# Performance work log

Hardware: AMD Instinct MI355X
Metric: run time of the kernel (lower is better)

Reference implementation:

```python
import jax, jax.numpy as jnp
import numpy as np

EPS_COS = 1e-8  # torch cosine_similarity eps
EPS_LN = 1e-5   # torch LayerNorm eps


def setup_inputs() -> dict:
    key = jax.random.key(0)
    ks = jax.random.split(key, 8)
    B, N, D, C = 256, 65536, 1024, 103
    s = 1.0 / np.sqrt(D)
    return {
        "visual_input": jnp.zeros((1,), jnp.float32),
        "query_input": jax.random.normal(ks[0], (B, D), jnp.float32),
        "memory_keys": jax.random.normal(ks[1], (N, D), jnp.float32),
        "W_enc": jax.random.normal(ks[2], (D, D), jnp.float32) * s,
        "b_enc": jnp.zeros((D,), jnp.float32),
        "W_d": jax.random.normal(ks[3], (D, D), jnp.float32) * s,
        "b_d": jnp.zeros((D,), jnp.float32),
        "ln_g": jnp.ones((D,), jnp.float32),
        "ln_b": jnp.zeros((D,), jnp.float32),
        "W_cls": jax.random.normal(ks[4], (C, 2 * D), jnp.float32) * (1.0 / np.sqrt(2 * D)),
        "b_cls": jnp.zeros((C,), jnp.float32),
        "k": 32,
    }


def reference(visual_input, query_input, memory_keys, W_enc, b_enc, W_d, b_d,
              ln_g, ln_b, W_cls, b_cls, k):
    # visual encoder + relu -> query embedding [B, D]
    q = jax.nn.relu(query_input @ W_enc.T + b_enc)
    # cosine-similarity kNN over memory bank [N, D]
    qn = q / jnp.maximum(jnp.linalg.norm(q, axis=-1, keepdims=True), EPS_COS)
    mn = memory_keys / jnp.maximum(jnp.linalg.norm(memory_keys, axis=-1, keepdims=True), EPS_COS)
    sim = qn @ mn.T                      # [B, N]
    _, idx = jax.lax.top_k(sim, k)       # [B, k]
    mk = memory_keys[idx]                # [B, k, D] gather
    # memory attention
    qt = jax.nn.relu(q @ W_d.T + b_d)    # [B, D]
    scores = jnp.einsum('bd,bkd->bk', qt, mk)
    w = jax.nn.softmax(scores, axis=-1)
    attended = jnp.einsum('bk,bkd->bd', w, mk)
    x = attended + q
    mu = jnp.mean(x, axis=-1, keepdims=True)
    var = jnp.mean((x - mu) ** 2, axis=-1, keepdims=True)
    ma_out = (x - mu) * jax.lax.rsqrt(var + EPS_LN) * ln_g + ln_b
    # classifier on concatenated features
    merged = jnp.concatenate([q, ma_out], axis=1)  # [B, 2D]
    return merged @ W_cls.T + b_cls
```

## Files before the change

### kernel.cpp

```cpp
#include <hip/hip_runtime.h>
#include <stdint.h>

typedef unsigned short u16;
typedef unsigned int u32;
typedef __attribute__((ext_vector_type(2))) float f32x2;
typedef __attribute__((ext_vector_type(4))) float f32x4;
typedef __attribute__((ext_vector_type(4))) u32 u32x4;
typedef __attribute__((ext_vector_type(2))) u32 u32x2;
typedef __attribute__((ext_vector_type(8))) short bf16x8;

#define NKEYS 65536
#define DIM 1024
#define BQ 256
#define NCLS 103
#define NCAND 64
#define SROW 40

__device__ __forceinline__ u16 f2bf(float x) {
  u32 u = __float_as_uint(x);
  u = u + 0x7FFFu + ((u >> 16) & 1u);
  return (u16)(u >> 16);
}
__device__ __forceinline__ u32 cvtpk(float lo, float hi) {
  u32 d;
  asm("v_cvt_pk_bf16_f32 %0, %1, %2" : "=v"(d) : "v"(lo), "v"(hi));
  return d;
}

__global__ __launch_bounds__(256) void gemm_nt_f32(
    const float* __restrict__ A, const float* __restrict__ B,
    float* __restrict__ partial)
{
  __shared__ float sAT[2][16][68];
  __shared__ float sBT[2][16][68];
  const int tid = threadIdx.x;
  const int n0 = blockIdx.x * 64;
  const int m0 = blockIdx.y * 64;
  const int kz = blockIdx.z;
  const int r = tid & 63, kq = tid >> 6;
  const int tx = tid & 15, ty = tid >> 4;
  float acc[4][4] = {};

  const float* ag = A + (size_t)(m0 + r) * DIM + kz * 256 + kq * 4;
  const float* bg = B + (size_t)(n0 + r) * DIM + kz * 256 + kq * 4;

  f32x4 av = *(const f32x4*)(ag);
  f32x4 bv = *(const f32x4*)(bg);
#pragma unroll
  for (int i = 0; i < 4; ++i) {
    sAT[0][kq * 4 + i][r] = av[i];
    sBT[0][kq * 4 + i][r] = bv[i];
  }
  __syncthreads();

  for (int kb = 0; kb < 16; ++kb) {
    const int cur = kb & 1;
    if (kb + 1 < 16) {
      av = *(const f32x4*)(ag + (kb + 1) * 16);
      bv = *(const f32x4*)(bg + (kb + 1) * 16);
    }
#pragma unroll
    for (int kk = 0; kk < 16; ++kk) {
      const f32x4 a4 = *(const f32x4*)&sAT[cur][kk][ty * 4];
      const f32x4 b4 = *(const f32x4*)&sBT[cur][kk][tx * 4];
#pragma unroll
      for (int i = 0; i < 4; ++i)
#pragma unroll
        for (int j = 0; j < 4; ++j) acc[i][j] += a4[i] * b4[j];
    }
    if (kb + 1 < 16) {
#pragma unroll
      for (int i = 0; i < 4; ++i) {
        sAT[cur ^ 1][kq * 4 + i][r] = av[i];
        sBT[cur ^ 1][kq * 4 + i][r] = bv[i];
      }
    }
    __syncthreads();
  }
#pragma unroll
  for (int i = 0; i < 4; ++i) {
    f32x4 ov = {acc[i][0], acc[i][1], acc[i][2], acc[i][3]};
    *(f32x4*)(partial + (size_t)kz * 262144u + (size_t)(m0 + ty * 4 + i) * DIM + n0 + tx * 4) = ov;
  }
}

__global__ __launch_bounds__(256) void reduce_bias_relu(
    const float* __restrict__ partial, const float* __restrict__ bias,
    float* __restrict__ outf, u16* __restrict__ outb, const int wbf)
{
  const int i4 = blockIdx.x * 256 + threadIdx.x;
  const int e = i4 * 4;
  const int n = e & (DIM - 1);
  f32x4 s = *(const f32x4*)(partial + e);
  s += *(const f32x4*)(partial + 262144u + e);
  s += *(const f32x4*)(partial + 2u * 262144u + e);
  s += *(const f32x4*)(partial + 3u * 262144u + e);
  s += *(const f32x4*)(bias + n);
#pragma unroll
  for (int i = 0; i < 4; ++i) s[i] = fmaxf(s[i], 0.f);
  *(f32x4*)(outf + e) = s;
  if (wbf) {
    u32x2 h = {cvtpk(s[0], s[1]), cvtpk(s[2], s[3])};
    *(u32x2*)(outb + e) = h;
  }
}

__global__ __launch_bounds__(512) void simgemm(
    const float* __restrict__ keys, const u16* __restrict__ qb,
    u16* __restrict__ sim)
{
  __shared__ u16 sA[2][256 * SROW];
  __shared__ u16 sB[2][128 * SROW];
  __shared__ float snorm[128];
  const int tid = threadIdx.x;
  const int n0 = blockIdx.x * 128;

  const int a_r = tid >> 1;
  const int a_h = (tid & 1) * 16;
  const u16* agp = qb + (size_t)a_r * DIM + a_h;
  const int a_ws = a_r * SROW + a_h;

  const int b_r = tid >> 2;
  const int b_q = (tid & 3) * 8;
  const float* bgp = keys + (size_t)(n0 + b_r) * DIM + b_q;
  const int b_ws = b_r * SROW + b_q;

  const int lane = tid & 63, wave = tid >> 6;
  const int wm = (wave >> 1) * 64;
  const int wn = (wave & 1) * 64;
  const int lr = lane & 15;
  const int lk = (lane >> 4) * 8;
  const int l4 = (lane >> 4) * 4;

  float nrm = 0.f;
  f32x4 acc[4][4];
#pragma unroll
  for (int i = 0; i < 4; ++i)
#pragma unroll
    for (int j = 0; j < 4; ++j) acc[i][j] = (f32x4){0.f, 0.f, 0.f, 0.f};

  f32x4 b00, b01, b10, b11, b20, b21, b30, b31;
  u32x4 a00, a01, a10, a11;

#define LOADB(B0, B1, T) do { \
    B0 = *(const f32x4*)(bgp + (size_t)(T) * 32); \
    B1 = *(const f32x4*)(bgp + (size_t)(T) * 32 + 4); \
  } while (0)
#define LOADA(A0, A1, T) do { \
    A0 = *(const u32x4*)(agp + (size_t)(T) * 32); \
    A1 = *(const u32x4*)(agp + (size_t)(T) * 32 + 8); \
  } while (0)
#define WRITE(B0, B1, A0, A1, BUF) do { \
    nrm += B0[0]*B0[0] + B0[1]*B0[1] + B0[2]*B0[2] + B0[3]*B0[3]; \
    nrm += B1[0]*B1[0] + B1[1]*B1[1] + B1[2]*B1[2] + B1[3]*B1[3]; \
    u32x4 bp; \
    bp.x = cvtpk(B0[0], B0[1]); bp.y = cvtpk(B0[2], B0[3]); \
    bp.z = cvtpk(B1[0], B1[1]); bp.w = cvtpk(B1[2], B1[3]); \
    *(u32x4*)&sB[BUF][b_ws] = bp; \
    *(u32x4*)&sA[BUF][a_ws] = A0; \
    *(u32x4*)&sA[BUF][a_ws + 8] = A1; \
  } while (0)
#define COMPUTE(BUF) do { \
    bf16x8 af[4], bfr[4]; \
    _Pragma("unroll") \
    for (int f = 0; f < 4; ++f) { \
      af[f]  = *(const bf16x8*)&sA[BUF][(wm + f * 16 + lr) * SROW + lk]; \
      bfr[f] = *(const bf16x8*)&sB[BUF][(wn + f * 16 + lr) * SROW + lk]; \
    } \
    _Pragma("unroll") \
    for (int i = 0; i < 4; ++i) \
      _Pragma("unroll") \
      for (int j = 0; j < 4; ++j) \
        acc[i][j] = __builtin_amdgcn_mfma_f32_16x16x32_bf16(af[i], bfr[j], acc[i][j], 0, 0, 0); \
  } while (0)

  LOADB(b00, b01, 0); LOADB(b10, b11, 1); LOADB(b20, b21, 2); LOADB(b30, b31, 3);
  LOADA(a00, a01, 0); LOADA(a10, a11, 1);
  WRITE(b00, b01, a00, a01, 0);
  __syncthreads();

  for (int tt = 0; tt < 32; tt += 4) {
    if (tt + 4 < 32) LOADB(b00, b01, tt + 4);
    LOADA(a00, a01, tt + 2);
    COMPUTE(0);
    WRITE(b10, b11, a10, a11, 1);
    __syncthreads();
    if (tt + 5 < 32) LOADB(b10, b11, tt + 5);
    LOADA(a10, a11, tt + 3);
    COMPUTE(1);
    WRITE(b20, b21, a00, a01, 0);
    __syncthreads();
    if (tt + 6 < 32) LOADB(b20, b21, tt + 6);
    if (tt + 4 < 32) LOADA(a00, a01, tt + 4);
    COMPUTE(0);
    WRITE(b30, b31, a10, a11, 1);
    __syncthreads();
    if (tt + 7 < 32) LOADB(b30, b31, tt + 7);
    if (tt + 5 < 32) LOADA(a10, a11, tt + 5);
    COMPUTE(1);
    if (tt + 4 < 32) WRITE(b00, b01, a00, a01, 0);
    __syncthreads();
  }
#undef LOADB
#undef LOADA
#undef WRITE
#undef COMPUTE

  nrm += __shfl_xor(nrm, 1);
  nrm += __shfl_xor(nrm, 2);
  if ((tid & 3) == 0) snorm[b_r] = nrm;
  __syncthreads();

#pragma unroll
  for (int j = 0; j < 4; ++j) {
    const int nl = wn + j * 16 + lr;
    const float scl = 1.f / fmaxf(sqrtf(snorm[nl]), 1e-8f);
    const size_t ng = (size_t)(n0 + nl);
#pragma unroll
    for (int i = 0; i < 4; ++i) {
      const int mb = wm + i * 16 + l4;
#pragma unroll
      for (int r = 0; r < 4; ++r) {
        sim[(size_t)(mb + r) * NKEYS + ng] = f2bf(acc[i][j][r] * scl);
      }
    }
  }
}

__global__ __launch_bounds__(512) void select_attn_cls(
    const u16* __restrict__ sim, const float* __restrict__ keys,
    const float* __restrict__ q, const float* __restrict__ qt,
    const float* __restrict__ ln_g, const float* __restrict__ ln_b,
    const float* __restrict__ Wc, const float* __restrict__ bc,
    float* __restrict__ out)
{
  __shared__ int redc[8];
  __shared__ int sc1, sc2;
  __shared__ int clist[NCAND];
  __shared__ float sdq[NCAND], sdqt[NCAND], snr[NCAND];
  __shared__ int srowi[32];
  __shared__ float sw[32];
  __shared__ float red1[8], red2[8];
  __shared__ float smg[2048];
  const int tid = threadIdx.x, lane = tid & 63, wave = tid >> 6;
  const int m = blockIdx.x;

  const u32x4* row = (const u32x4*)(sim + (size_t)m * NKEYS);
  u32 ku[16][4];
#pragma unroll
  for (int i = 0; i < 16; ++i) {
    const u32x4 v = row[i * 512 + tid];
#pragma unroll
    for (int c = 0; c < 4; ++c) {
      u32 lo = v[c] & 0xFFFFu, hi = v[c] >> 16;
      lo ^= (lo & 0x8000u) ? 0xFFFFu : 0x8000u;
      hi ^= (hi & 0x8000u) ? 0xFFFFu : 0x8000u;
      ku[i][c] = lo | (hi << 16);
    }
  }
  int lo_b = 0, hi_b = 65536;
  while (hi_b - lo_b > 1) {
    const u32 mid = (u32)((lo_b + hi_b) >> 1);
    int c = 0;
#pragma unroll
    for (int i = 0; i < 16; ++i)
#pragma unroll
      for (int k = 0; k < 4; ++k) {
        const u32 x = ku[i][k];
        c += ((x & 0xFFFFu) >= mid) ? 1 : 0;
        c += ((x >> 16) >= mid) ? 1 : 0;
      }
#pragma unroll
    for (int j = 32; j; j >>= 1) c += __shfl_xor(c, j);
    if ((tid & 63) == 0) redc[tid >> 6] = c;
    __syncthreads();
    int tot = 0;
#pragma unroll
    for (int w = 0; w < 8; ++w) tot += redc[w];
    if (tot >= NCAND) lo_b = (int)mid; else hi_b = (int)mid;
    __syncthreads();
  }
  const u32 tau = (u32)lo_b;

  int ch = 0;
#pragma unroll
  for (int i = 0; i < 16; ++i)
#pragma unroll
    for (int k = 0; k < 4; ++k) {
      const u32 x = ku[i][k];
      ch += ((x & 0xFFFFu) > tau) ? 1 : 0;
      ch += ((x >> 16) > tau) ? 1 : 0;
    }
#pragma unroll
  for (int j = 32; j; j >>= 1) ch += __shfl_xor(ch, j);
  if ((tid & 63) == 0) redc[tid >> 6] = ch;
  if (tid == 0) { sc1 = 0; sc2 = 0; }
  __syncthreads();
  int nhi = 0;
#pragma unroll
  for (int w = 0; w < 8; ++w) nhi += redc[w];

#pragma unroll
  for (int i = 0; i < 16; ++i)
#pragma unroll
    for (int k = 0; k < 4; ++k) {
      const int nb = (i * 512 + tid) * 8 + k * 2;
      const u32 x = ku[i][k];
      const u32 l = x & 0xFFFFu, h = x >> 16;
      if (l > tau) { int p = atomicAdd(&sc1, 1); clist[p] = nb; }
      else if (l == tau) { int p = atomicAdd(&sc2, 1); if (nhi + p < NCAND) clist[nhi + p] = nb; }
      if (h > tau) { int p = atomicAdd(&sc1, 1); clist[p] = nb + 1; }
      else if (h == tau) { int p = atomicAdd(&sc2, 1); if (nhi + p < NCAND) clist[nhi + p] = nb + 1; }
    }
  __syncthreads();

  f32x4 q4[4], qt4[4];
#pragma unroll
  for (int i = 0; i < 4; ++i) {
    q4[i]  = *(const f32x4*)(q  + (size_t)m * DIM + i * 256 + lane * 4);
    qt4[i] = *(const f32x4*)(qt + (size_t)m * DIM + i * 256 + lane * 4);
  }
  for (int ci = 0; ci < 8; ++ci) {
    const int c = wave * 8 + ci;
    const float* kr = keys + (size_t)clist[c] * DIM;
    float dq = 0.f, dt = 0.f, ss = 0.f;
#pragma unroll
    for (int i = 0; i < 4; ++i) {
      const f32x4 kv = *(const f32x4*)(kr + i * 256 + lane * 4);
#pragma unroll
      for (int e = 0; e < 4; ++e) {
        dq += kv[e] * q4[i][e];
        dt += kv[e] * qt4[i][e];
        ss += kv[e] * kv[e];
      }
    }
#pragma unroll
    for (int j = 32; j; j >>= 1) {
      dq += __shfl_xor(dq, j);
      dt += __shfl_xor(dt, j);
      ss += __shfl_xor(ss, j);
    }
    if (lane == 0) { sdq[c] = dq; sdqt[c] = dt; snr[c] = ss; }
  }
  __syncthreads();

  if (wave == 0) {
    float v = sdq[lane] / fmaxf(sqrtf(snr[lane]), 1e-8f);
    int p = lane;
#pragma unroll
    for (int k = 2; k <= 64; k <<= 1)
#pragma unroll
      for (int j = k >> 1; j > 0; j >>= 1) {
        const float ov = __shfl_xor(v, j);
        const int op = __shfl_xor(p, j);
        const bool tl = ((lane & j) == 0) == ((lane & k) == 0);
        const bool take = tl ? (ov > v) : (ov < v);
        if (take) { v = ov; p = op; }
      }
    float sc = (lane < 32) ? sdqt[p] : -3.4e38f;
    float mx = sc;
#pragma unroll
    for (int j = 16; j; j >>= 1) mx = fmaxf(mx, __shfl_xor(mx, j));
    const float e = (lane < 32) ? expf(sc - mx) : 0.f;
    float s = e;
#pragma unroll
    for (int j = 16; j; j >>= 1) s += __shfl_xor(s, j);
    if (lane < 32) { sw[lane] = e / s; srowi[lane] = clist[p]; }
  }
  __syncthreads();

  const int d0 = tid * 2;
  f32x2 at = {0.f, 0.f};
  for (int j = 0; j < 32; ++j) {
    const float wj = sw[j];
    const f32x2 kv = *(const f32x2*)(keys + (size_t)srowi[j] * DIM + d0);
    at += wj * kv;
  }
  const f32x2 qv = *(const f32x2*)(q + (size_t)m * DIM + d0);
  const f32x2 x = at + qv;
  float s1 = x[0] + x[1];
#pragma unroll
  for (int j = 32; j; j >>= 1) s1 += __shfl_xor(s1, j);
  if (lane == 0) red1[wave] = s1;
  __syncthreads();
  float mu = 0.f;
#pragma unroll
  for (int w = 0; w < 8; ++w) mu += red1[w];
  mu *= (1.f / 1024.f);
  const f32x2 xc = x - mu;
  float s2 = xc[0] * xc[0] + xc[1] * xc[1];
#pragma unroll
  for (int j = 32; j; j >>= 1) s2 += __shfl_xor(s2, j);
  if (lane == 0) red2[wave] = s2;
  __syncthreads();
  float var = 0.f;
#pragma unroll
  for (int w = 0; w < 8; ++w) var += red2[w];
  var *= (1.f / 1024.f);
  const float rstd = rsqrtf(var + 1e-5f);
  const f32x2 g = *(const f32x2*)(ln_g + d0);
  const f32x2 b = *(const f32x2*)(ln_b + d0);
  const f32x2 ma = xc * rstd * g + b;
  *(f32x2*)&smg[d0] = qv;
  *(f32x2*)&smg[1024 + d0] = ma;
  __syncthreads();

  for (int c = wave; c < NCLS; c += 8) {
    const float* w = Wc + (size_t)c * 2048;
    float a = 0.f;
#pragma unroll
    for (int i = 0; i < 8; ++i) {
      const f32x4 wv = *(const f32x4*)(w + i * 256 + lane * 4);
      const f32x4 mv = *(const f32x4*)&smg[i * 256 + lane * 4];
#pragma unroll
      for (int e = 0; e < 4; ++e) a += wv[e] * mv[e];
    }
#pragma unroll
    for (int j = 32; j; j >>= 1) a += __shfl_xor(a, j);
    if (lane == 0) out[(size_t)m * NCLS + c] = a + bc[c];
  }
}

extern "C" void kernel_launch(void* const* d_in, const int* in_sizes, int n_in,
                              void* d_out, int out_size, void* d_ws, size_t ws_size,
                              hipStream_t stream)
{
  const float* query = (const float*)d_in[1];
  const float* keys  = (const float*)d_in[2];
  const float* Wenc  = (const float*)d_in[3];
  const float* benc  = (const float*)d_in[4];
  const float* Wd    = (const float*)d_in[5];
  const float* bd    = (const float*)d_in[6];
  const float* lng   = (const float*)d_in[7];
  const float* lnb   = (const float*)d_in[8];
  const float* Wcls  = (const float*)d_in[9];
  const float* bcls  = (const float*)d_in[10];
  float* out = (float*)d_out;
  char* ws = (char*)d_ws;

  float* q   = (float*)(ws + 0);
  float* qt  = (float*)(ws + 1048576u);
  u16*   qb  = (u16*)(ws + 2097152u);
  char*  big = ws + 2621440u;
  float* par = (float*)big;
  u16*   sim = (u16*)big;

  gemm_nt_f32<<<dim3(16, 4, 4), 256, 0, stream>>>(query, Wenc, par);
  reduce_bias_relu<<<256, 256, 0, stream>>>(par, benc, q, qb, 1);
  gemm_nt_f32<<<dim3(16, 4, 4), 256, 0, stream>>>(q, Wd, par);
  reduce_bias_relu<<<256, 256, 0, stream>>>(par, bd, qt, qb, 0);
  simgemm<<<dim3(512), 512, 0, stream>>>(keys, qb, sim);
  select_attn_cls<<<256, 512, 0, stream>>>(sim, keys, q, qt, lng, lnb, Wcls, bcls, out);
}
```

Before: 183.5 us.

## Fuse all stages into one persistent kernel with software grid barriers

```diff
diff --git a/kernel.cpp b/kernel.cpp
--- a/kernel.cpp
+++ b/kernel.cpp
@@ -11,10 +11,11 @@
 
 #define NKEYS 65536
 #define DIM 1024
-#define BQ 256
 #define NCLS 103
 #define NCAND 64
 #define SROW 40
+#define NBLK 256
+#define NTHR 512
 
 __device__ __forceinline__ u16 f2bf(float x) {
   u32 u = __float_as_uint(x);
@@ -27,120 +28,160 @@
   return d;
 }
 
-__global__ __launch_bounds__(256) void gemm_nt_f32(
-    const float* __restrict__ A, const float* __restrict__ B,
-    float* __restrict__ partial)
+union SMEM {
+  struct { float sAT[2][32][68]; float sBT[2][32][68]; } g;
+  struct { u16 sA[2][256 * SROW]; u16 sB[2][128 * SROW]; float snorm[128]; } s;
+  struct { int redc[8]; int sc1, sc2; int clist[NCAND];
+           float sdq[NCAND], sdqt[NCAND], snr[NCAND];
+           int srowi[32]; float sw[32]; float red1[8], red2[8];
+           float smg[2048]; } t;
+};
+
+__device__ __forceinline__ void gridbar(u32* cnt, u32* gen) {
+  __syncthreads();
+  if (threadIdx.x == 0) {
+    __threadfence();
+    u32 g0 = __hip_atomic_load(gen, __ATOMIC_RELAXED, __HIP_MEMORY_SCOPE_AGENT);
+    u32 old = __hip_atomic_fetch_add(cnt, 1u, __ATOMIC_ACQ_REL, __HIP_MEMORY_SCOPE_AGENT);
+    if (old == NBLK - 1u) {
+      __hip_atomic_store(cnt, 0u, __ATOMIC_RELAXED, __HIP_MEMORY_SCOPE_AGENT);
+      __hip_atomic_fetch_add(gen, 1u, __ATOMIC_ACQ_REL, __HIP_MEMORY_SCOPE_AGENT);
+    } else {
+      while (__hip_atomic_load(gen, __ATOMIC_ACQUIRE, __HIP_MEMORY_SCOPE_AGENT) == g0)
+        __builtin_amdgcn_s_sleep(2);
+    }
+    __threadfence();
+  }
+  __syncthreads();
+}
+
+__device__ __forceinline__ void small_gemm(const float* __restrict__ A,
+                                           const float* __restrict__ B,
+                                           float* __restrict__ partial,
+                                           SMEM* sm, int b, int tid) {
+  const int n0 = (b & 15) * 64;
+  const int m0 = ((b >> 4) & 3) * 64;
+  const int kz = (b >> 6) & 3;
+  const int ar = tid & 63;
+  const int kq = (tid >> 6) * 4;
+  const int tx = tid & 15, ty = tid >> 4;
+  float acc[2][4] = {};
+  const float* ag = A + (size_t)(m0 + ar) * DIM + kz * 256 + kq;
+  const float* bg = B + (size_t)(n0 + ar) * DIM + kz * 256 + kq;
+  f32x4 av = *(const f32x4*)ag;
+  f32x4 bv = *(const f32x4*)bg;
+#pragma unroll
+  for (int i = 0; i < 4; ++i) {
+    sm->g.sAT[0][kq + i][ar] = av[i];
+    sm->g.sBT[0][kq + i][ar] = bv[i];
+  }
+  __syncthreads();
+  for (int kb = 0; kb < 8; ++kb) {
+    const int cur = kb & 1;
+    if (kb + 1 < 8) {
+      av = *(const f32x4*)(ag + (kb + 1) * 32);
+      bv = *(const f32x4*)(bg + (kb + 1) * 32);
+    }
+#pragma unroll
+    for (int kk = 0; kk < 32; ++kk) {
+      const f32x2 a2 = *(const f32x2*)&sm->g.sAT[cur][kk][ty * 2];
+      const f32x4 b4 = *(const f32x4*)&sm->g.sBT[cur][kk][tx * 4];
+#pragma unroll
+      for (int i = 0; i < 2; ++i)
+#pragma unroll
+        for (int j = 0; j < 4; ++j) acc[i][j] += a2[i] * b4[j];
+    }
+    if (kb + 1 < 8) {
+#pragma unroll
+      for (int i = 0; i < 4; ++i) {
+        sm->g.sAT[cur ^ 1][kq + i][ar] = av[i];
+        sm->g.sBT[cur ^ 1][kq + i][ar] = bv[i];
+      }
+    }
+    __syncthreads();
+  }
+#pragma unroll
+  for (int i = 0; i < 2; ++i) {
+    f32x4 ov = {acc[i][0], acc[i][1], acc[i][2], acc[i][3]};
+    *(f32x4*)(partial + (size_t)kz * 262144u + (size_t)(m0 + ty * 2 + i) * DIM + n0 + tx * 4) = ov;
+  }
+}
+
+__device__ __forceinline__ void reduce_phase(const float* __restrict__ partial,
+                                             const float* __restrict__ bias,
+                                             float* __restrict__ outf,
+                                             u16* __restrict__ outb, int gid) {
+  if (gid < 65536) {
+    const int e = gid * 4;
+    const int n = e & (DIM - 1);
+    f32x4 s = *(const f32x4*)(partial + e);
+    s += *(const f32x4*)(partial + 262144u + e);
+    s += *(const f32x4*)(partial + 2u * 262144u + e);
+    s += *(const f32x4*)(partial + 3u * 262144u + e);
+    s += *(const f32x4*)(bias + n);
+#pragma unroll
+    for (int i = 0; i < 4; ++i) s[i] = fmaxf(s[i], 0.f);
+    *(f32x4*)(outf + e) = s;
+    if (outb) {
+      u32x2 h = {cvtpk(s[0], s[1]), cvtpk(s[2], s[3])};
+      *(u32x2*)(outb + e) = h;
+    }
+  }
+}
+
+__global__ __launch_bounds__(NTHR, 2) void mega(
+    const float* __restrict__ query, const float* __restrict__ keys,
+    const float* __restrict__ Wenc, const float* __restrict__ benc,
+    const float* __restrict__ Wd, const float* __restrict__ bd,
+    const float* __restrict__ lng, const float* __restrict__ lnb,
+    const float* __restrict__ Wc, const float* __restrict__ bc,
+    float* __restrict__ q, float* __restrict__ qt, u16* __restrict__ qb,
+    float* __restrict__ par1, float* __restrict__ par2, u16* __restrict__ sim,
+    u32* __restrict__ bar, float* __restrict__ out)
 {
-  __shared__ float sAT[2][16][68];
-  __shared__ float sBT[2][16][68];
+  __shared__ SMEM smem;
+  SMEM* const sm = &smem;
   const int tid = threadIdx.x;
-  const int n0 = blockIdx.x * 64;
-  const int m0 = blockIdx.y * 64;
-  const int kz = blockIdx.z;
-  const int r = tid & 63, kq = tid >> 6;
-  const int tx = tid & 15, ty = tid >> 4;
-  float acc[4][4] = {};
-
-  const float* ag = A + (size_t)(m0 + r) * DIM + kz * 256 + kq * 4;
-  const float* bg = B + (size_t)(n0 + r) * DIM + kz * 256 + kq * 4;
-
-  f32x4 av = *(const f32x4*)(ag);
-  f32x4 bv = *(const f32x4*)(bg);
-#pragma unroll
-  for (int i = 0; i < 4; ++i) {
-    sAT[0][kq * 4 + i][r] = av[i];
-    sBT[0][kq * 4 + i][r] = bv[i];
-  }
-  __syncthreads();
-
-  for (int kb = 0; kb < 16; ++kb) {
-    const int cur = kb & 1;
-    if (kb + 1 < 16) {
-      av = *(const f32x4*)(ag + (kb + 1) * 16);
-      bv = *(const f32x4*)(bg + (kb + 1) * 16);
-    }
-#pragma unroll
-    for (int kk = 0; kk < 16; ++kk) {
-      const f32x4 a4 = *(const f32x4*)&sAT[cur][kk][ty * 4];
-      const f32x4 b4 = *(const f32x4*)&sBT[cur][kk][tx * 4];
+  const int b = blockIdx.x;
+  const int lane = tid & 63, wave = tid >> 6;
+  u32* cnt = bar;
+  u32* gen = bar + 32;
+
+  small_gemm(query, Wenc, par1, sm, b, tid);
+  gridbar(cnt, gen);
+  reduce_phase(par1, benc, q, qb, b * NTHR + tid);
+  gridbar(cnt, gen);
+  small_gemm(q, Wd, par2, sm, b, tid);
+  gridbar(cnt, gen);
+  reduce_phase(par2, bd, qt, (u16*)0, b * NTHR + tid);
+  gridbar(cnt, gen);
+
+  {
+    const int a_r = tid >> 1;
+    const int a_h = (tid & 1) * 16;
+    const u16* agp = qb + (size_t)a_r * DIM + a_h;
+    const int a_ws = a_r * SROW + a_h;
+    const int b_r = tid >> 2;
+    const int b_q = (tid & 3) * 8;
+    const int b_ws = b_r * SROW + b_q;
+    const int wm = (wave >> 1) * 64;
+    const int wn = (wave & 1) * 64;
+    const int lr = lane & 15;
+    const int lk = (lane >> 4) * 8;
+    const int l4 = (lane >> 4) * 4;
+
+    for (int s = 0; s < 2; ++s) {
+      const int n0 = (b * 2 + s) * 128;
+      const float* bgp = keys + (size_t)(n0 + b_r) * DIM + b_q;
+      float nrm = 0.f;
+      f32x4 acc[4][4];
 #pragma unroll
       for (int i = 0; i < 4; ++i)
 #pragma unroll
-        for (int j = 0; j < 4; ++j) acc[i][j] += a4[i] * b4[j];
-    }
-    if (kb + 1 < 16) {
-#pragma unroll
-      for (int i = 0; i < 4; ++i) {
-        sAT[cur ^ 1][kq * 4 + i][r] = av[i];
-        sBT[cur ^ 1][kq * 4 + i][r] = bv[i];
-      }
-    }
-    __syncthreads();
-  }
-#pragma unroll
-  for (int i = 0; i < 4; ++i) {
-    f32x4 ov = {acc[i][0], acc[i][1], acc[i][2], acc[i][3]};
-    *(f32x4*)(partial + (size_t)kz * 262144u + (size_t)(m0 + ty * 4 + i) * DIM + n0 + tx * 4) = ov;
-  }
-}
-
-__global__ __launch_bounds__(256) void reduce_bias_relu(
-    const float* __restrict__ partial, const float* __restrict__ bias,
-    float* __restrict__ outf, u16* __restrict__ outb, const int wbf)
-{
-  const int i4 = blockIdx.x * 256 + threadIdx.x;
-  const int e = i4 * 4;
-  const int n = e & (DIM - 1);
-  f32x4 s = *(const f32x4*)(partial + e);
-  s += *(const f32x4*)(partial + 262144u + e);
-  s += *(const f32x4*)(partial + 2u * 262144u + e);
-  s += *(const f32x4*)(partial + 3u * 262144u + e);
-  s += *(const f32x4*)(bias + n);
-#pragma unroll
-  for (int i = 0; i < 4; ++i) s[i] = fmaxf(s[i], 0.f);
-  *(f32x4*)(outf + e) = s;
-  if (wbf) {
-    u32x2 h = {cvtpk(s[0], s[1]), cvtpk(s[2], s[3])};
-    *(u32x2*)(outb + e) = h;
-  }
-}
-
-__global__ __launch_bounds__(512) void simgemm(
-    const float* __restrict__ keys, const u16* __restrict__ qb,
-    u16* __restrict__ sim)
-{
-  __shared__ u16 sA[2][256 * SROW];
-  __shared__ u16 sB[2][128 * SROW];
-  __shared__ float snorm[128];
-  const int tid = threadIdx.x;
-  const int n0 = blockIdx.x * 128;
-
-  const int a_r = tid >> 1;
-  const int a_h = (tid & 1) * 16;
-  const u16* agp = qb + (size_t)a_r * DIM + a_h;
-  const int a_ws = a_r * SROW + a_h;
-
-  const int b_r = tid >> 2;
-  const int b_q = (tid & 3) * 8;
-  const float* bgp = keys + (size_t)(n0 + b_r) * DIM + b_q;
-  const int b_ws = b_r * SROW + b_q;
-
-  const int lane = tid & 63, wave = tid >> 6;
-  const int wm = (wave >> 1) * 64;
-  const int wn = (wave & 1) * 64;
-  const int lr = lane & 15;
-  const int lk = (lane >> 4) * 8;
-  const int l4 = (lane >> 4) * 4;
-
-  float nrm = 0.f;
-  f32x4 acc[4][4];
-#pragma unroll
-  for (int i = 0; i < 4; ++i)
-#pragma unroll
-    for (int j = 0; j < 4; ++j) acc[i][j] = (f32x4){0.f, 0.f, 0.f, 0.f};
-
-  f32x4 b00, b01, b10, b11, b20, b21, b30, b31;
-  u32x4 a00, a01, a10, a11;
+        for (int j = 0; j < 4; ++j) acc[i][j] = (f32x4){0.f, 0.f, 0.f, 0.f};
+
+      f32x4 b00, b01, b10, b11, b20, b21, b30, b31;
+      u32x4 a00, a01, a10, a11;
 
 #define LOADB(B0, B1, T) do { \
     B0 = *(const f32x4*)(bgp + (size_t)(T) * 32); \
@@ -156,16 +197,16 @@
     u32x4 bp; \
     bp.x = cvtpk(B0[0], B0[1]); bp.y = cvtpk(B0[2], B0[3]); \
     bp.z = cvtpk(B1[0], B1[1]); bp.w = cvtpk(B1[2], B1[3]); \
-    *(u32x4*)&sB[BUF][b_ws] = bp; \
-    *(u32x4*)&sA[BUF][a_ws] = A0; \
-    *(u32x4*)&sA[BUF][a_ws + 8] = A1; \
+    *(u32x4*)&sm->s.sB[BUF][b_ws] = bp; \
+    *(u32x4*)&sm->s.sA[BUF][a_ws] = A0; \
+    *(u32x4*)&sm->s.sA[BUF][a_ws + 8] = A1; \
   } while (0)
 #define COMPUTE(BUF) do { \
     bf16x8 af[4], bfr[4]; \
     _Pragma("unroll") \
     for (int f = 0; f < 4; ++f) { \
-      af[f]  = *(const bf16x8*)&sA[BUF][(wm + f * 16 + lr) * SROW + lk]; \
-      bfr[f] = *(const bf16x8*)&sB[BUF][(wn + f * 16 + lr) * SROW + lk]; \
+      af[f]  = *(const bf16x8*)&sm->s.sA[BUF][(wm + f * 16 + lr) * SROW + lk]; \
+      bfr[f] = *(const bf16x8*)&sm->s.sB[BUF][(wn + f * 16 + lr) * SROW + lk]; \
     } \
     _Pragma("unroll") \
     for (int i = 0; i < 4; ++i) \
@@ -174,250 +215,238 @@
         acc[i][j] = __builtin_amdgcn_mfma_f32_16x16x32_bf16(af[i], bfr[j], acc[i][j], 0, 0, 0); \
   } while (0)
 
-  LOADB(b00, b01, 0); LOADB(b10, b11, 1); LOADB(b20, b21, 2); LOADB(b30, b31, 3);
-  LOADA(a00, a01, 0); LOADA(a10, a11, 1);
-  WRITE(b00, b01, a00, a01, 0);
-  __syncthreads();
-
-  for (int tt = 0; tt < 32; tt += 4) {
-    if (tt + 4 < 32) LOADB(b00, b01, tt + 4);
-    LOADA(a00, a01, tt + 2);
-    COMPUTE(0);
-    WRITE(b10, b11, a10, a11, 1);
-    __syncthreads();
-    if (tt + 5 < 32) LOADB(b10, b11, tt + 5);
-    LOADA(a10, a11, tt + 3);
-    COMPUTE(1);
-    WRITE(b20, b21, a00, a01, 0);
-    __syncthreads();
-    if (tt + 6 < 32) LOADB(b20, b21, tt + 6);
-    if (tt + 4 < 32) LOADA(a00, a01, tt + 4);
-    COMPUTE(0);
-    WRITE(b30, b31, a10, a11, 1);
-    __syncthreads();
-    if (tt + 7 < 32) LOADB(b30, b31, tt + 7);
-    if (tt + 5 < 32) LOADA(a10, a11, tt + 5);
-    COMPUTE(1);
-    if (tt + 4 < 32) WRITE(b00, b01, a00, a01, 0);
-    __syncthreads();
-  }
+      LOADB(b00, b01, 0); LOADB(b10, b11, 1); LOADB(b20, b21, 2); LOADB(b30, b31, 3);
+      LOADA(a00, a01, 0); LOADA(a10, a11, 1);
+      WRITE(b00, b01, a00, a01, 0);
+      __syncthreads();
+
+      for (int tt = 0; tt < 32; tt += 4) {
+        if (tt + 4 < 32) LOADB(b00, b01, tt + 4);
+        LOADA(a00, a01, tt + 2);
+        COMPUTE(0);
+        WRITE(b10, b11, a10, a11, 1);
+        __syncthreads();
+        if (tt + 5 < 32) LOADB(b10, b11, tt + 5);
+        LOADA(a10, a11, tt + 3);
+        COMPUTE(1);
+        WRITE(b20, b21, a00, a01, 0);
+        __syncthreads();
+        if (tt + 6 < 32) LOADB(b20, b21, tt + 6);
+        if (tt + 4 < 32) LOADA(a00, a01, tt + 4);
+        COMPUTE(0);
+        WRITE(b30, b31, a10, a11, 1);
+        __syncthreads();
+        if (tt + 7 < 32) LOADB(b30, b31, tt + 7);
+        if (tt + 5 < 32) LOADA(a10, a11, tt + 5);
+        COMPUTE(1);
+        if (tt + 4 < 32) WRITE(b00, b01, a00, a01, 0);
+        __syncthreads();
+      }
 #undef LOADB
 #undef LOADA
 #undef WRITE
 #undef COMPUTE
 
-  nrm += __shfl_xor(nrm, 1);
-  nrm += __shfl_xor(nrm, 2);
-  if ((tid & 3) == 0) snorm[b_r] = nrm;
-  __syncthreads();
-
-#pragma unroll
-  for (int j = 0; j < 4; ++j) {
-    const int nl = wn + j * 16 + lr;
-    const float scl = 1.f / fmaxf(sqrtf(snorm[nl]), 1e-8f);
-    const size_t ng = (size_t)(n0 + nl);
-#pragma unroll
-    for (int i = 0; i < 4; ++i) {
-      const int mb = wm + i * 16 + l4;
-#pragma unroll
-      for (int r = 0; r < 4; ++r) {
-        sim[(size_t)(mb + r) * NKEYS + ng] = f2bf(acc[i][j][r] * scl);
-      }
-    }
-  }
-}
-
-__global__ __launch_bounds__(512) void select_attn_cls(
-    const u16* __restrict__ sim, const float* __restrict__ keys,
-    const float* __restrict__ q, const float* __restrict__ qt,
-    const float* __restrict__ ln_g, const float* __restrict__ ln_b,
-    const float* __restrict__ Wc, const float* __restrict__ bc,
-    float* __restrict__ out)
-{
-  __shared__ int redc[8];
-  __shared__ int sc1, sc2;
-  __shared__ int clist[NCAND];
-  __shared__ float sdq[NCAND], sdqt[NCAND], snr[NCAND];
-  __shared__ int srowi[32];
-  __shared__ float sw[32];
-  __shared__ float red1[8], red2[8];
-  __shared__ float smg[2048];
-  const int tid = threadIdx.x, lane = tid & 63, wave = tid >> 6;
-  const int m = blockIdx.x;
-
-  const u32x4* row = (const u32x4*)(sim + (size_t)m * NKEYS);
-  u32 ku[16][4];
-#pragma unroll
-  for (int i = 0; i < 16; ++i) {
-    const u32x4 v = row[i * 512 + tid];
-#pragma unroll
-    for (int c = 0; c < 4; ++c) {
-      u32 lo = v[c] & 0xFFFFu, hi = v[c] >> 16;
-      lo ^= (lo & 0x8000u) ? 0xFFFFu : 0x8000u;
-      hi ^= (hi & 0x8000u) ? 0xFFFFu : 0x8000u;
-      ku[i][c] = lo | (hi << 16);
-    }
-  }
-  int lo_b = 0, hi_b = 65536;
-  while (hi_b - lo_b > 1) {
-    const u32 mid = (u32)((lo_b + hi_b) >> 1);
-    int c = 0;
+      nrm += __shfl_xor(nrm, 1);
+      nrm += __shfl_xor(nrm, 2);
+      if ((tid & 3) == 0) sm->s.snorm[b_r] = nrm;
+      __syncthreads();
+
+#pragma unroll
+      for (int j = 0; j < 4; ++j) {
+        const int nl = wn + j * 16 + lr;
+        const float scl = 1.f / fmaxf(sqrtf(sm->s.snorm[nl]), 1e-8f);
+        const size_t ng = (size_t)(n0 + nl);
+#pragma unroll
+        for (int i = 0; i < 4; ++i) {
+          const int mb = wm + i * 16 + l4;
+#pragma unroll
+          for (int r = 0; r < 4; ++r) {
+            sim[(size_t)(mb + r) * NKEYS + ng] = f2bf(acc[i][j][r] * scl);
+          }
+        }
+      }
+      __syncthreads();
+    }
+  }
+  gridbar(cnt, gen);
+
+  {
+    const int m = b;
+    const u32x4* row = (const u32x4*)(sim + (size_t)m * NKEYS);
+    u32 ku[16][4];
+#pragma unroll
+    for (int i = 0; i < 16; ++i) {
+      const u32x4 v = row[i * 512 + tid];
+#pragma unroll
+      for (int c = 0; c < 4; ++c) {
+        u32 lo = v[c] & 0xFFFFu, hi = v[c] >> 16;
+        lo ^= (lo & 0x8000u) ? 0xFFFFu : 0x8000u;
+        hi ^= (hi & 0x8000u) ? 0xFFFFu : 0x8000u;
+        ku[i][c] = lo | (hi << 16);
+      }
+    }
+    int lo_b = 0, hi_b = 65536;
+    while (hi_b - lo_b > 1) {
+      const u32 mid = (u32)((lo_b + hi_b) >> 1);
+      int c = 0;
+#pragma unroll
+      for (int i = 0; i < 16; ++i)
+#pragma unroll
+        for (int k = 0; k < 4; ++k) {
+          const u32 x = ku[i][k];
+          c += ((x & 0xFFFFu) >= mid) ? 1 : 0;
+          c += ((x >> 16) >= mid) ? 1 : 0;
+        }
+#pragma unroll
+      for (int j = 32; j; j >>= 1) c += __shfl_xor(c, j);
+      if ((tid & 63) == 0) sm->t.redc[tid >> 6] = c;
+      __syncthreads();
+      int tot = 0;
+#pragma unroll
+      for (int w = 0; w < 8; ++w) tot += sm->t.redc[w];
+      if (tot >= NCAND) lo_b = (int)mid; else hi_b = (int)mid;
+      __syncthreads();
+    }
+    const u32 tau = (u32)lo_b;
+
+    int ch = 0;
 #pragma unroll
     for (int i = 0; i < 16; ++i)
 #pragma unroll
       for (int k = 0; k < 4; ++k) {
         const u32 x = ku[i][k];
-        c += ((x & 0xFFFFu) >= mid) ? 1 : 0;
-        c += ((x >> 16) >= mid) ? 1 : 0;
-      }
-#pragma unroll
-    for (int j = 32; j; j >>= 1) c += __shfl_xor(c, j);
-    if ((tid & 63) == 0) redc[tid >> 6] = c;
-    __syncthreads();
-    int tot = 0;
-#pragma unroll
-    for (int w = 0; w < 8; ++w) tot += redc[w];
-    if (tot >= NCAND) lo_b = (int)mid; else hi_b = (int)mid;
-    __syncthreads();
-  }
-  const u32 tau = (u32)lo_b;
-
-  int ch = 0;
-#pragma unroll
-  for (int i = 0; i < 16; ++i)
-#pragma unroll
-    for (int k = 0; k < 4; ++k) {
-      const u32 x = ku[i][k];
-      ch += ((x & 0xFFFFu) > tau) ? 1 : 0;
-      ch += ((x >> 16) > tau) ? 1 : 0;
-    }
-#pragma unroll
-  for (int j = 32; j; j >>= 1) ch += __shfl_xor(ch, j);
-  if ((tid & 63) == 0) redc[tid >> 6] = ch;
-  if (tid == 0) { sc1 = 0; sc2 = 0; }
-  __syncthreads();
-  int nhi = 0;
-#pragma unroll
-  for (int w = 0; w < 8; ++w) nhi += redc[w];
-
-#pragma unroll
-  for (int i = 0; i < 16; ++i)
-#pragma unroll
-    for (int k = 0; k < 4; ++k) {
-      const int nb = (i * 512 + tid) * 8 + k * 2;
-      const u32 x = ku[i][k];
-      const u32 l = x & 0xFFFFu, h = x >> 16;
-      if (l > tau) { int p = atomicAdd(&sc1, 1); clist[p] = nb; }
-      else if (l == tau) { int p = atomicAdd(&sc2, 1); if (nhi + p < NCAND) clist[nhi + p] = nb; }
-      if (h > tau) { int p = atomicAdd(&sc1, 1); clist[p] = nb + 1; }
-      else if (h == tau) { int p = atomicAdd(&sc2, 1); if (nhi + p < NCAND) clist[nhi + p] = nb + 1; }
-    }
-  __syncthreads();
-
-  f32x4 q4[4], qt4[4];
-#pragma unroll
-  for (int i = 0; i < 4; ++i) {
-    q4[i]  = *(const f32x4*)(q  + (size_t)m * DIM + i * 256 + lane * 4);
-    qt4[i] = *(const f32x4*)(qt + (size_t)m * DIM + i * 256 + lane * 4);
-  }
-  for (int ci = 0; ci < 8; ++ci) {
-    const int c = wave * 8 + ci;
-    const float* kr = keys + (size_t)clist[c] * DIM;
-    float dq = 0.f, dt = 0.f, ss = 0.f;
+        ch += ((x & 0xFFFFu) > tau) ? 1 : 0;
+        ch += ((x >> 16) > tau) ? 1 : 0;
+      }
+#pragma unroll
+    for (int j = 32; j; j >>= 1) ch += __shfl_xor(ch, j);
+    if ((tid & 63) == 0) sm->t.redc[tid >> 6] = ch;
+    if (tid == 0) { sm->t.sc1 = 0; sm->t.sc2 = 0; }
+    __syncthreads();
+    int nhi = 0;
+#pragma unroll
+    for (int w = 0; w < 8; ++w) nhi += sm->t.redc[w];
+
+#pragma unroll
+    for (int i = 0; i < 16; ++i)
+#pragma unroll
+      for (int k = 0; k < 4; ++k) {
+        const int nb = (i * 512 + tid) * 8 + k * 2;
+        const u32 x = ku[i][k];
+        const u32 l = x & 0xFFFFu, h = x >> 16;
+        if (l > tau) { int p = atomicAdd(&sm->t.sc1, 1); sm->t.clist[p] = nb; }
+        else if (l == tau) { int p = atomicAdd(&sm->t.sc2, 1); if (nhi + p < NCAND) sm->t.clist[nhi + p] = nb; }
+        if (h > tau) { int p = atomicAdd(&sm->t.sc1, 1); sm->t.clist[p] = nb + 1; }
+        else if (h == tau) { int p = atomicAdd(&sm->t.sc2, 1); if (nhi + p < NCAND) sm->t.clist[nhi + p] = nb + 1; }
+      }
+    __syncthreads();
+
+    f32x4 q4[4], qt4[4];
 #pragma unroll
     for (int i = 0; i < 4; ++i) {
-      const f32x4 kv = *(const f32x4*)(kr + i * 256 + lane * 4);
-#pragma unroll
-      for (int e = 0; e < 4; ++e) {
-        dq += kv[e] * q4[i][e];
-        dt += kv[e] * qt4[i][e];
-        ss += kv[e] * kv[e];
-      }
-    }
-#pragma unroll
-    for (int j = 32; j; j >>= 1) {
-      dq += __shfl_xor(dq, j);
-      dt += __shfl_xor(dt, j);
-      ss += __shfl_xor(ss, j);
-    }
-    if (lane == 0) { sdq[c] = dq; sdqt[c] = dt; snr[c] = ss; }
-  }
-  __syncthreads();
-
-  if (wave == 0) {
-    float v = sdq[lane] / fmaxf(sqrtf(snr[lane]), 1e-8f);
-    int p = lane;
-#pragma unroll
-    for (int k = 2; k <= 64; k <<= 1)
-#pragma unroll
-      for (int j = k >> 1; j > 0; j >>= 1) {
-        const float ov = __shfl_xor(v, j);
-        const int op = __shfl_xor(p, j);
-        const bool tl = ((lane & j) == 0) == ((lane & k) == 0);
-        const bool take = tl ? (ov > v) : (ov < v);
-        if (take) { v = ov; p = op; }
-      }
-    float sc = (lane < 32) ? sdqt[p] : -3.4e38f;
-    float mx = sc;
-#pragma unroll
-    for (int j = 16; j; j >>= 1) mx = fmaxf(mx, __shfl_xor(mx, j));
-    const float e = (lane < 32) ? expf(sc - mx) : 0.f;
-    float s = e;
-#pragma unroll
-    for (int j = 16; j; j >>= 1) s += __shfl_xor(s, j);
-    if (lane < 32) { sw[lane] = e / s; srowi[lane] = clist[p]; }
-  }
-  __syncthreads();
-
-  const int d0 = tid * 2;
-  f32x2 at = {0.f, 0.f};
-  for (int j = 0; j < 32; ++j) {
-    const float wj = sw[j];
-    const f32x2 kv = *(const f32x2*)(keys + (size_t)srowi[j] * DIM + d0);
-    at += wj * kv;
-  }
-  const f32x2 qv = *(const f32x2*)(q + (size_t)m * DIM + d0);
-  const f32x2 x = at + qv;
-  float s1 = x[0] + x[1];
-#pragma unroll
-  for (int j = 32; j; j >>= 1) s1 += __shfl_xor(s1, j);
-  if (lane == 0) red1[wave] = s1;
-  __syncthreads();
-  float mu = 0.f;
-#pragma unroll
-  for (int w = 0; w < 8; ++w) mu += red1[w];
-  mu *= (1.f / 1024.f);
-  const f32x2 xc = x - mu;
-  float s2 = xc[0] * xc[0] + xc[1] * xc[1];
-#pragma unroll
-  for (int j = 32; j; j >>= 1) s2 += __shfl_xor(s2, j);
-  if (lane == 0) red2[wave] = s2;
-  __syncthreads();
-  float var = 0.f;
-#pragma unroll
-  for (int w = 0; w < 8; ++w) var += red2[w];
-  var *= (1.f / 1024.f);
-  const float rstd = rsqrtf(var + 1e-5f);
-  const f32x2 g = *(const f32x2*)(ln_g + d0);
-  const f32x2 b = *(const f32x2*)(ln_b + d0);
-  const f32x2 ma = xc * rstd * g + b;
-  *(f32x2*)&smg[d0] = qv;
-  *(f32x2*)&smg[1024 + d0] = ma;
-  __syncthreads();
-
-  for (int c = wave; c < NCLS; c += 8) {
-    const float* w = Wc + (size_t)c * 2048;
-    float a = 0.f;
-#pragma unroll
-    for (int i = 0; i < 8; ++i) {
-      const f32x4 wv = *(const f32x4*)(w + i * 256 + lane * 4);
-      const f32x4 mv = *(const f32x4*)&smg[i * 256 + lane * 4];
-#pragma unroll
-      for (int e = 0; e < 4; ++e) a += wv[e] * mv[e];
-    }
-#pragma unroll
-    for (int j = 32; j; j >>= 1) a += __shfl_xor(a, j);
-    if (lane == 0) out[(size_t)m * NCLS + c] = a + bc[c];
+      q4[i]  = *(const f32x4*)(q  + (size_t)m * DIM + i * 256 + lane * 4);
+      qt4[i] = *(const f32x4*)(qt + (size_t)m * DIM + i * 256 + lane * 4);
+    }
+    for (int ci = 0; ci < 8; ++ci) {
+      const int c = wave * 8 + ci;
+      const float* kr = keys + (size_t)sm->t.clist[c] * DIM;
+      float dq = 0.f, dt = 0.f, ss = 0.f;
+#pragma unroll
+      for (int i = 0; i < 4; ++i) {
+        const f32x4 kv = *(const f32x4*)(kr + i * 256 + lane * 4);
+#pragma unroll
+        for (int e = 0; e < 4; ++e) {
+          dq += kv[e] * q4[i][e];
+          dt += kv[e] * qt4[i][e];
+          ss += kv[e] * kv[e];
+        }
+      }
+#pragma unroll
+      for (int j = 32; j; j >>= 1) {
+        dq += __shfl_xor(dq, j);
+        dt += __shfl_xor(dt, j);
+        ss += __shfl_xor(ss, j);
+      }
+      if (lane == 0) { sm->t.sdq[c] = dq; sm->t.sdqt[c] = dt; sm->t.snr[c] = ss; }
+    }
+    __syncthreads();
+
+    if (wave == 0) {
+      float v = sm->t.sdq[lane] / fmaxf(sqrtf(sm->t.snr[lane]), 1e-8f);
+      int p = lane;
+#pragma unroll
+      for (int k = 2; k <= 64; k <<= 1)
+#pragma unroll
+        for (int j = k >> 1; j > 0; j >>= 1) {
+          const float ov = __shfl_xor(v, j);
+          const int op = __shfl_xor(p, j);
+          const bool tl = ((lane & j) == 0) == ((lane & k) == 0);
+          const bool take = tl ? (ov > v) : (ov < v);
+          if (take) { v = ov; p = op; }
+        }
+      float sc = (lane < 32) ? sm->t.sdqt[p] : -3.4e38f;
+      float mx = sc;
+#pragma unroll
+      for (int j = 16; j; j >>= 1) mx = fmaxf(mx, __shfl_xor(mx, j));
+      const float e = (lane < 32) ? expf(sc - mx) : 0.f;
+      float ssum = e;
+#pragma unroll
+      for (int j = 16; j; j >>= 1) ssum += __shfl_xor(ssum, j);
+      if (lane < 32) { sm->t.sw[lane] = e / ssum; sm->t.srowi[lane] = sm->t.clist[p]; }
+    }
+    __syncthreads();
+
+    const int d0 = tid * 2;
+    f32x2 at = {0.f, 0.f};
+    for (int j = 0; j < 32; ++j) {
+      const float wj = sm->t.sw[j];
+      const f32x2 kv = *(const f32x2*)(keys + (size_t)sm->t.srowi[j] * DIM + d0);
+      at += wj * kv;
+    }
+    const f32x2 qv = *(const f32x2*)(q + (size_t)m * DIM + d0);
+    const f32x2 x = at + qv;
+    float s1 = x[0] + x[1];
+#pragma unroll
+    for (int j = 32; j; j >>= 1) s1 += __shfl_xor(s1, j);
+    if (lane == 0) sm->t.red1[wave] = s1;
+    __syncthreads();
+    float mu = 0.f;
+#pragma unroll
+    for (int w = 0; w < 8; ++w) mu += sm->t.red1[w];
+    mu *= (1.f / 1024.f);
+    const f32x2 xc = x - mu;
+    float s2 = xc[0] * xc[0] + xc[1] * xc[1];
+#pragma unroll
+    for (int j = 32; j; j >>= 1) s2 += __shfl_xor(s2, j);
+    if (lane == 0) sm->t.red2[wave] = s2;
+    __syncthreads();
+    float var = 0.f;
+#pragma unroll
+    for (int w = 0; w < 8; ++w) var += sm->t.red2[w];
+    var *= (1.f / 1024.f);
+    const float rstd = rsqrtf(var + 1e-5f);
+    const f32x2 g = *(const f32x2*)(lng + d0);
+    const f32x2 bb = *(const f32x2*)(lnb + d0);
+    const f32x2 ma = xc * rstd * g + bb;
+    *(f32x2*)&sm->t.smg[d0] = qv;
+    *(f32x2*)&sm->t.smg[1024 + d0] = ma;
+    __syncthreads();
+
+    for (int c = wave; c < NCLS; c += 8) {
+      const float* w = Wc + (size_t)c * 2048;
+      float a = 0.f;
+#pragma unroll
+      for (int i = 0; i < 8; ++i) {
+        const f32x4 wv = *(const f32x4*)(w + i * 256 + lane * 4);
+        const f32x4 mv = *(const f32x4*)&sm->t.smg[i * 256 + lane * 4];
+#pragma unroll
+        for (int e = 0; e < 4; ++e) a += wv[e] * mv[e];
+      }
+#pragma unroll
+      for (int j = 32; j; j >>= 1) a += __shfl_xor(a, j);
+      if (lane == 0) out[(size_t)m * NCLS + c] = a + bc[c];
+    }
   }
 }
 
@@ -441,14 +470,13 @@
   float* q   = (float*)(ws + 0);
   float* qt  = (float*)(ws + 1048576u);
   u16*   qb  = (u16*)(ws + 2097152u);
-  char*  big = ws + 2621440u;
-  float* par = (float*)big;
+  u32*   bar = (u32*)(ws + 2621440u);
+  char*  big = ws + 2625536u;
   u16*   sim = (u16*)big;
-
-  gemm_nt_f32<<<dim3(16, 4, 4), 256, 0, stream>>>(query, Wenc, par);
-  reduce_bias_relu<<<256, 256, 0, stream>>>(par, benc, q, qb, 1);
-  gemm_nt_f32<<<dim3(16, 4, 4), 256, 0, stream>>>(q, Wd, par);
-  reduce_bias_relu<<<256, 256, 0, stream>>>(par, bd, qt, qb, 0);
-  simgemm<<<dim3(512), 512, 0, stream>>>(keys, qb, sim);
-  select_attn_cls<<<256, 512, 0, stream>>>(sim, keys, q, qt, lng, lnb, Wcls, bcls, out);
-}
+  float* par1 = (float*)big;
+  float* par2 = (float*)(big + 4194304u);
+
+  hipMemsetAsync(bar, 0, 256, stream);
+  mega<<<NBLK, NTHR, 0, stream>>>(query, keys, Wenc, benc, Wd, bd, lng, lnb,
+                                  Wcls, bcls, q, qt, qb, par1, par2, sim, bar, out);
+}
```

New measurement: 365.3 us. 1.99x slower.

## Fuse encoder GEMMs and reductions into one persistent kernel with grid barriers

Applied to the files above, without the earlier changes.

```diff
diff --git a/kernel.cpp b/kernel.cpp
--- a/kernel.cpp
+++ b/kernel.cpp
@@ -11,10 +11,10 @@
 
 #define NKEYS 65536
 #define DIM 1024
-#define BQ 256
 #define NCLS 103
 #define NCAND 64
 #define SROW 40
+#define NBLK 256
 
 __device__ __forceinline__ u16 f2bf(float x) {
   u32 u = __float_as_uint(x);
@@ -27,82 +27,112 @@
   return d;
 }
 
-__global__ __launch_bounds__(256) void gemm_nt_f32(
-    const float* __restrict__ A, const float* __restrict__ B,
-    float* __restrict__ partial)
+__device__ __forceinline__ void gridbar(u32* cnt, u32* gen) {
+  __syncthreads();
+  if (threadIdx.x == 0) {
+    __threadfence();
+    u32 g0 = __hip_atomic_load(gen, __ATOMIC_RELAXED, __HIP_MEMORY_SCOPE_AGENT);
+    u32 old = __hip_atomic_fetch_add(cnt, 1u, __ATOMIC_ACQ_REL, __HIP_MEMORY_SCOPE_AGENT);
+    if (old == NBLK - 1u) {
+      __hip_atomic_store(cnt, 0u, __ATOMIC_RELAXED, __HIP_MEMORY_SCOPE_AGENT);
+      __hip_atomic_fetch_add(gen, 1u, __ATOMIC_ACQ_REL, __HIP_MEMORY_SCOPE_AGENT);
+    } else {
+      while (__hip_atomic_load(gen, __ATOMIC_ACQUIRE, __HIP_MEMORY_SCOPE_AGENT) == g0)
+        __builtin_amdgcn_s_sleep(2);
+    }
+    __threadfence();
+  }
+  __syncthreads();
+}
+
+__device__ __forceinline__ void small_gemm(const float* __restrict__ A,
+                                           const float* __restrict__ B,
+                                           float* __restrict__ partial,
+                                           float (&sAT)[2][32][68],
+                                           float (&sBT)[2][32][68],
+                                           int b, int tid) {
+  const int n0 = (b & 15) * 64;
+  const int m0 = ((b >> 4) & 3) * 64;
+  const int kz = (b >> 6) & 3;
+  const int ar = tid & 63;
+  const int kq = (tid >> 6) * 4;
+  const int tx = tid & 15, ty = tid >> 4;
+  float acc[2][4] = {};
+  const float* ag = A + (size_t)(m0 + ar) * DIM + kz * 256 + kq;
+  const float* bg = B + (size_t)(n0 + ar) * DIM + kz * 256 + kq;
+  f32x4 av = *(const f32x4*)ag;
+  f32x4 bv = *(const f32x4*)bg;
+#pragma unroll
+  for (int i = 0; i < 4; ++i) {
+    sAT[0][kq + i][ar] = av[i];
+    sBT[0][kq + i][ar] = bv[i];
+  }
+  __syncthreads();
+  for (int kb = 0; kb < 8; ++kb) {
+    const int cur = kb & 1;
+    if (kb + 1 < 8) {
+      av = *(const f32x4*)(ag + (kb + 1) * 32);
+      bv = *(const f32x4*)(bg + (kb + 1) * 32);
+    }
+#pragma unroll
+    for (int kk = 0; kk < 32; ++kk) {
+      const f32x2 a2 = *(const f32x2*)&sAT[cur][kk][ty * 2];
+      const f32x4 b4 = *(const f32x4*)&sBT[cur][kk][tx * 4];
+#pragma unroll
+      for (int i = 0; i < 2; ++i)
+#pragma unroll
+        for (int j = 0; j < 4; ++j) acc[i][j] += a2[i] * b4[j];
+    }
+    if (kb + 1 < 8) {
+#pragma unroll
+      for (int i = 0; i < 4; ++i) {
+        sAT[cur ^ 1][kq + i][ar] = av[i];
+        sBT[cur ^ 1][kq + i][ar] = bv[i];
+      }
+    }
+    __syncthreads();
+  }
+#pragma unroll
+  for (int i = 0; i < 2; ++i) {
+    f32x4 ov = {acc[i][0], acc[i][1], acc[i][2], acc[i][3]};
+    *(f32x4*)(partial + (size_t)kz * 262144u + (size_t)(m0 + ty * 2 + i) * DIM + n0 + tx * 4) = ov;
+  }
+}
+
+__device__ __forceinline__ void reduce_phase(const float* __restrict__ partial,
+                                             const float* __restrict__ bias,
+                                             float* __restrict__ outf,
+                                             u16* __restrict__ outb, int gid) {
+  const int e = gid * 2;
+  const int n = e & (DIM - 1);
+  f32x2 s = *(const f32x2*)(partial + e);
+  s += *(const f32x2*)(partial + 262144u + e);
+  s += *(const f32x2*)(partial + 2u * 262144u + e);
+  s += *(const f32x2*)(partial + 3u * 262144u + e);
+  s += *(const f32x2*)(bias + n);
+  s[0] = fmaxf(s[0], 0.f);
+  s[1] = fmaxf(s[1], 0.f);
+  *(f32x2*)(outf + e) = s;
+  if (outb) {
+    u32 h = cvtpk(s[0], s[1]);
+    *(u32*)(outb + e) = h;
+  }
+}
+
+__global__ __launch_bounds__(512) void pipe12(
+    const float* __restrict__ query, const float* __restrict__ Wenc,
+    const float* __restrict__ benc, const float* __restrict__ Wd,
+    float* __restrict__ q, u16* __restrict__ qb,
+    float* __restrict__ par1, float* __restrict__ par2, u32* __restrict__ bar)
 {
-  __shared__ float sAT[2][16][68];
-  __shared__ float sBT[2][16][68];
-  const int tid = threadIdx.x;
-  const int n0 = blockIdx.x * 64;
-  const int m0 = blockIdx.y * 64;
-  const int kz = blockIdx.z;
-  const int r = tid & 63, kq = tid >> 6;
-  const int tx = tid & 15, ty = tid >> 4;
-  float acc[4][4] = {};
-
-  const float* ag = A + (size_t)(m0 + r) * DIM + kz * 256 + kq * 4;
-  const float* bg = B + (size_t)(n0 + r) * DIM + kz * 256 + kq * 4;
-
-  f32x4 av = *(const f32x4*)(ag);
-  f32x4 bv = *(const f32x4*)(bg);
-#pragma unroll
-  for (int i = 0; i < 4; ++i) {
-    sAT[0][kq * 4 + i][r] = av[i];
-    sBT[0][kq * 4 + i][r] = bv[i];
-  }
-  __syncthreads();
-
-  for (int kb = 0; kb < 16; ++kb) {
-    const int cur = kb & 1;
-    if (kb + 1 < 16) {
-      av = *(const f32x4*)(ag + (kb + 1) * 16);
-      bv = *(const f32x4*)(bg + (kb + 1) * 16);
-    }
-#pragma unroll
-    for (int kk = 0; kk < 16; ++kk) {
-      const f32x4 a4 = *(const f32x4*)&sAT[cur][kk][ty * 4];
-      const f32x4 b4 = *(const f32x4*)&sBT[cur][kk][tx * 4];
-#pragma unroll
-      for (int i = 0; i < 4; ++i)
-#pragma unroll
-        for (int j = 0; j < 4; ++j) acc[i][j] += a4[i] * b4[j];
-    }
-    if (kb + 1 < 16) {
-#pragma unroll
-      for (int i = 0; i < 4; ++i) {
-        sAT[cur ^ 1][kq * 4 + i][r] = av[i];
-        sBT[cur ^ 1][kq * 4 + i][r] = bv[i];
-      }
-    }
-    __syncthreads();
-  }
-#pragma unroll
-  for (int i = 0; i < 4; ++i) {
-    f32x4 ov = {acc[i][0], acc[i][1], acc[i][2], acc[i][3]};
-    *(f32x4*)(partial + (size_t)kz * 262144u + (size_t)(m0 + ty * 4 + i) * DIM + n0 + tx * 4) = ov;
-  }
-}
-
-__global__ __launch_bounds__(256) void reduce_bias_relu(
-    const float* __restrict__ partial, const float* __restrict__ bias,
-    float* __restrict__ outf, u16* __restrict__ outb, const int wbf)
-{
-  const int i4 = blockIdx.x * 256 + threadIdx.x;
-  const int e = i4 * 4;
-  const int n = e & (DIM - 1);
-  f32x4 s = *(const f32x4*)(partial + e);
-  s += *(const f32x4*)(partial + 262144u + e);
-  s += *(const f32x4*)(partial + 2u * 262144u + e);
-  s += *(const f32x4*)(partial + 3u * 262144u + e);
-  s += *(const f32x4*)(bias + n);
-#pragma unroll
-  for (int i = 0; i < 4; ++i) s[i] = fmaxf(s[i], 0.f);
-  *(f32x4*)(outf + e) = s;
-  if (wbf) {
-    u32x2 h = {cvtpk(s[0], s[1]), cvtpk(s[2], s[3])};
-    *(u32x2*)(outb + e) = h;
-  }
+  __shared__ float sAT[2][32][68];
+  __shared__ float sBT[2][32][68];
+  const int tid = threadIdx.x, b = blockIdx.x;
+  small_gemm(query, Wenc, par1, sAT, sBT, b, tid);
+  gridbar(bar, bar + 32);
+  reduce_phase(par1, benc, q, qb, b * 512 + tid);
+  gridbar(bar, bar + 32);
+  small_gemm(q, Wd, par2, sAT, sBT, b, tid);
 }
 
 __global__ __launch_bounds__(512) void simgemm(
@@ -227,13 +257,16 @@
   }
 }
 
-__global__ __launch_bounds__(512) void select_attn_cls(
+__global__ __launch_bounds__(512) void selqt(
     const u16* __restrict__ sim, const float* __restrict__ keys,
-    const float* __restrict__ q, const float* __restrict__ qt,
+    const float* __restrict__ q, const float* __restrict__ par2,
+    const float* __restrict__ bd,
     const float* __restrict__ ln_g, const float* __restrict__ ln_b,
     const float* __restrict__ Wc, const float* __restrict__ bc,
     float* __restrict__ out)
 {
+  __shared__ float sqt[DIM];
+  __shared__ float smg[2048];
   __shared__ int redc[8];
   __shared__ int sc1, sc2;
   __shared__ int clist[NCAND];
@@ -241,9 +274,20 @@
   __shared__ int srowi[32];
   __shared__ float sw[32];
   __shared__ float red1[8], red2[8];
-  __shared__ float smg[2048];
   const int tid = threadIdx.x, lane = tid & 63, wave = tid >> 6;
   const int m = blockIdx.x;
+
+  {
+    const int e = tid * 2;
+    f32x2 s = *(const f32x2*)(par2 + (size_t)m * DIM + e);
+    s += *(const f32x2*)(par2 + 262144u + (size_t)m * DIM + e);
+    s += *(const f32x2*)(par2 + 2u * 262144u + (size_t)m * DIM + e);
+    s += *(const f32x2*)(par2 + 3u * 262144u + (size_t)m * DIM + e);
+    s += *(const f32x2*)(bd + e);
+    sqt[e]     = fmaxf(s[0], 0.f);
+    sqt[e + 1] = fmaxf(s[1], 0.f);
+  }
+  __syncthreads();
 
   const u32x4* row = (const u32x4*)(sim + (size_t)m * NKEYS);
   u32 ku[16][4];
@@ -317,8 +361,8 @@
   f32x4 q4[4], qt4[4];
 #pragma unroll
   for (int i = 0; i < 4; ++i) {
-    q4[i]  = *(const f32x4*)(q  + (size_t)m * DIM + i * 256 + lane * 4);
-    qt4[i] = *(const f32x4*)(qt + (size_t)m * DIM + i * 256 + lane * 4);
+    q4[i]  = *(const f32x4*)(q + (size_t)m * DIM + i * 256 + lane * 4);
+    qt4[i] = *(const f32x4*)&sqt[i * 256 + lane * 4];
   }
   for (int ci = 0; ci < 8; ++ci) {
     const int c = wave * 8 + ci;
@@ -399,8 +443,8 @@
   var *= (1.f / 1024.f);
   const float rstd = rsqrtf(var + 1e-5f);
   const f32x2 g = *(const f32x2*)(ln_g + d0);
-  const f32x2 b = *(const f32x2*)(ln_b + d0);
-  const f32x2 ma = xc * rstd * g + b;
+  const f32x2 bb = *(const f32x2*)(ln_b + d0);
+  const f32x2 ma = xc * rstd * g + bb;
   *(f32x2*)&smg[d0] = qv;
   *(f32x2*)&smg[1024 + d0] = ma;
   __syncthreads();
@@ -438,17 +482,16 @@
   float* out = (float*)d_out;
   char* ws = (char*)d_ws;
 
-  float* q   = (float*)(ws + 0);
-  float* qt  = (float*)(ws + 1048576u);
-  u16*   qb  = (u16*)(ws + 2097152u);
-  char*  big = ws + 2621440u;
-  float* par = (float*)big;
-  u16*   sim = (u16*)big;
-
-  gemm_nt_f32<<<dim3(16, 4, 4), 256, 0, stream>>>(query, Wenc, par);
-  reduce_bias_relu<<<256, 256, 0, stream>>>(par, benc, q, qb, 1);
-  gemm_nt_f32<<<dim3(16, 4, 4), 256, 0, stream>>>(q, Wd, par);
-  reduce_bias_relu<<<256, 256, 0, stream>>>(par, bd, qt, qb, 0);
-  simgemm<<<dim3(512), 512, 0, stream>>>(keys, qb, sim);
-  select_attn_cls<<<256, 512, 0, stream>>>(sim, keys, q, qt, lng, lnb, Wcls, bcls, out);
-}
+  float* q    = (float*)(ws + 0);
+  u16*   qb   = (u16*)(ws + 1048576u);
+  u32*   bar  = (u32*)(ws + 1572864u);
+  char*  big  = ws + 1576960u;
+  u16*   sim  = (u16*)big;
+  float* par1 = (float*)big;
+  float* par2 = (float*)(ws + 35131392u);
+
+  hipMemsetAsync(bar, 0, 256, stream);
+  pipe12<<<NBLK, 512, 0, stream>>>(query, Wenc, benc, Wd, q, qb, par1, par2, bar);
+  simgemm<<<512, 512, 0, stream>>>(keys, qb, sim);
+  selqt<<<NBLK, 512, 0, stream>>>(sim, keys, q, par2, bd, lng, lnb, Wcls, bcls, out);
+}
```

Measured after the change: 237.8 us. 1.3x slower.
